# Kernel optimization log

Hardware: AMD Instinct MI355X
Metric: run time of the kernel (lower is better)

The kernel has to match this reference:

```python
import jax, jax.numpy as jnp
import numpy as np

N_NODES = 100000
N_EDGES = 1600000
D_IN = 64
HID = 64
N_GRAPHS = 256


def _glorot(key, shape):
    lim = float(np.sqrt(6.0 / (shape[0] + shape[1])))
    return jax.random.uniform(key, shape, jnp.float32, -lim, lim)


def setup_inputs() -> dict:
    key = jax.random.key(0)
    ks = jax.random.split(key, 12)
    x = jax.random.normal(ks[0], (N_NODES, D_IN), jnp.float32)
    edge_index = jax.random.randint(ks[1], (2, N_EDGES), 0, N_NODES, jnp.int64)
    batch = jnp.sort(jax.random.randint(ks[2], (N_NODES,), 0, N_GRAPHS, jnp.int64))
    params = {
        'Wrel1': _glorot(ks[3], (D_IN, HID)), 'brel1': jnp.zeros((HID,), jnp.float32), 'Wroot1': _glorot(ks[4], (D_IN, HID)),
        'Wrel2': _glorot(ks[5], (HID, HID)), 'brel2': jnp.zeros((HID,), jnp.float32), 'Wroot2': _glorot(ks[6], (HID, HID)),
        'Wrel3': _glorot(ks[7], (HID, HID)), 'brel3': jnp.zeros((HID,), jnp.float32), 'Wroot3': _glorot(ks[8], (HID, HID)),
        'Wlin': _glorot(ks[9], (HID, HID)), 'blin': jnp.zeros((HID,), jnp.float32),
    }
    return {'x': x, 'edge_index': edge_index, 'batch': batch, **params}


def _graph_conv(x, src, dst, Wrel, brel, Wroot):
    # PyG GraphConv: lin_rel(sum_{j in N(i)} x_j) + lin_root(x_i); bias on lin_rel only.
    aggr = jax.ops.segment_sum(x[src], dst, num_segments=N_NODES)  # [N, d] gather+scatter-add
    return aggr @ Wrel + brel + x @ Wroot


def reference(x, edge_index, batch, Wrel1, brel1, Wroot1, Wrel2, brel2, Wroot2,
              Wrel3, brel3, Wroot3, Wlin, blin):
    src, dst = edge_index[0], edge_index[1]
    h = jax.nn.relu(_graph_conv(x, src, dst, Wrel1, brel1, Wroot1))
    h = jax.nn.relu(_graph_conv(h, src, dst, Wrel2, brel2, Wroot2))
    h = _graph_conv(h, src, dst, Wrel3, brel3, Wroot3)
    # global_mean_pool over graphs
    sums = jax.ops.segment_sum(h, batch, num_segments=N_GRAPHS)          # [G, HID]
    counts = jax.ops.segment_sum(jnp.ones((N_NODES,), h.dtype), batch, num_segments=N_GRAPHS)
    pooled = sums / jnp.maximum(counts, 1.0)[:, None]
    # dropout is identity in eval mode
    return pooled @ Wlin + blin
```

## Files before the change

kernel.cpp:

```cpp
#include <hip/hip_runtime.h>
#include <hip/hip_bf16.h>

#define NN 100000
#define NE 1600000
#define DD 64
#define NG 256
#define SHIFT 8
#define NBK 391
#define BCAP 4608
#define NSB 256
#define CHUNK 6250

typedef __attribute__((ext_vector_type(8))) short bf16x8;
typedef __attribute__((ext_vector_type(4))) float f32x4;
typedef __attribute__((ext_vector_type(8))) unsigned short ushort8v;

__device__ __forceinline__ float b2f(ushort u){
  unsigned v = ((unsigned)u) << 16;
  return __uint_as_float(v);
}
__device__ __forceinline__ ushort f2b(float f){
  __hip_bfloat16 b = __float2bfloat16(f);
  return *(ushort*)&b;
}

__global__ void k_wpack3(const float* __restrict__ Wr1, const float* __restrict__ Wo1,
                         const float* __restrict__ Wr2, const float* __restrict__ Wo2,
                         const float* __restrict__ Wr3, const float* __restrict__ Wo3,
                         ushort* __restrict__ wp, int* __restrict__ gcur){
  int i = blockIdx.x*256 + threadIdx.x;
  if (i < NBK) gcur[i] = i*BCAP;
  if (i >= 3*8192) return;
  int lay = i >> 13;
  int r = i & 8191;
  int j = r & 7, l = (r>>3) & 63, t = (r>>9) & 7, s = r >> 12;
  int k = s*32 + ((l>>4)<<3) + j;
  int col = t*16 + (l&15);
  const float* Wrel  = (lay==0) ? Wr1 : (lay==1) ? Wr2 : Wr3;
  const float* Wroot = (lay==0) ? Wo1 : (lay==1) ? Wo2 : Wo3;
  float v = (col < 64) ? Wrel[k*64 + col] : Wroot[k*64 + (col-64)];
  wp[i] = f2b(v);
}

__global__ __launch_bounds__(256) void k_bscatter(const int* __restrict__ src, const int* __restrict__ dst,
                           int* __restrict__ gcur, unsigned* __restrict__ ebuf){
  __shared__ int h[NBK];
  __shared__ int base[NBK];
  __shared__ int lcur[NBK];
  for (int i=threadIdx.x; i<NBK; i+=256) h[i]=0;
  __syncthreads();
  const int e0 = blockIdx.x*CHUNK;
  const int e1 = min(e0+CHUNK, NE);
  for (int e=e0+threadIdx.x; e<e1; e+=256) atomicAdd(&h[dst[e]>>SHIFT], 1);
  __syncthreads();
  for (int i=threadIdx.x; i<NBK; i+=256){
    base[i] = h[i] ? atomicAdd(&gcur[i], h[i]) : 0;
    lcur[i] = 0;
  }
  __syncthreads();
  for (int e=e0+threadIdx.x; e<e1; e+=256){
    int d = dst[e];
    int b = d >> SHIFT;
    int r = atomicAdd(&lcur[b], 1);
    size_t idx = (size_t)base[b] + r;
    if (idx < (size_t)NBK*BCAP)
      ebuf[idx] = ((unsigned)(d & 255) << 17) | (unsigned)src[e];
  }
}

__global__ __launch_bounds__(256) void k_bfill(const unsigned* __restrict__ ebuf, const int* __restrict__ gcur,
                        int* __restrict__ rowptr, int* __restrict__ degarr, int* __restrict__ csr){
  __shared__ int c[256];
  __shared__ int lcur[256];
  __shared__ int s[256];
  __shared__ int scnt;
  const int b = blockIdx.x, t = threadIdx.x;
  const int ebase = b*BCAP;
  if (t == 0) scnt = min(gcur[b] - ebase, BCAP);
  c[t] = 0;
  __syncthreads();
  const int cnt = scnt;
  for (int i=t; i<cnt; i+=256) atomicAdd(&c[ebuf[ebase+i]>>17], 1);
  __syncthreads();
  int v = c[t];
  s[t] = v;
  __syncthreads();
  for (int off=1; off<256; off<<=1){
    int u = (t >= off) ? s[t-off] : 0;
    __syncthreads();
    s[t] += u;
    __syncthreads();
  }
  int excl = s[t] - v;
  lcur[t] = excl;
  int node = (b << SHIFT) + t;
  if (node < NN){ rowptr[node] = ebase + excl; degarr[node] = v; }
  __syncthreads();
  for (int i=t; i<cnt; i+=256){
    unsigned p = ebuf[ebase+i];
    int dl = (int)(p >> 17);
    int r = atomicAdd(&lcur[dl], 1);
    csr[ebase + r] = (int)(p & 0x1FFFFu);
  }
}

#define CPAD 136
__global__ __launch_bounds__(256) void k_gemm_mfma(const void* __restrict__ Av, int aIsF32,
    const ushort* __restrict__ wp, ushort* __restrict__ Y, ushort* __restrict__ Rr){
  __shared__ ushort ct[64*CPAD];
  const int tid = threadIdx.x;
  const int w = tid >> 6, l = tid & 63;
  const int m = l & 15, kg = l >> 4;
  const int row0 = blockIdx.x*64;
  int arow = row0 + w*16 + m; if (arow >= NN) arow = NN-1;
  bf16x8 a0, a1;
  if (aIsF32){
    const float* Af = (const float*)Av;
    float4 f0 = *(const float4*)&Af[(size_t)arow*64 + kg*8];
    float4 f1 = *(const float4*)&Af[(size_t)arow*64 + kg*8 + 4];
    float4 f2 = *(const float4*)&Af[(size_t)arow*64 + 32 + kg*8];
    float4 f3 = *(const float4*)&Af[(size_t)arow*64 + 32 + kg*8 + 4];
    a0[0]=(short)f2b(f0.x); a0[1]=(short)f2b(f0.y); a0[2]=(short)f2b(f0.z); a0[3]=(short)f2b(f0.w);
    a0[4]=(short)f2b(f1.x); a0[5]=(short)f2b(f1.y); a0[6]=(short)f2b(f1.z); a0[7]=(short)f2b(f1.w);
    a1[0]=(short)f2b(f2.x); a1[1]=(short)f2b(f2.y); a1[2]=(short)f2b(f2.z); a1[3]=(short)f2b(f2.w);
    a1[4]=(short)f2b(f3.x); a1[5]=(short)f2b(f3.y); a1[6]=(short)f2b(f3.z); a1[7]=(short)f2b(f3.w);
  } else {
    const ushort* Ab = (const ushort*)Av;
    a0 = *(const bf16x8*)&Ab[(size_t)arow*64 + kg*8];
    a1 = *(const bf16x8*)&Ab[(size_t)arow*64 + 32 + kg*8];
  }
  #pragma unroll
  for (int t=0; t<8; t++){
    bf16x8 b0 = *(const bf16x8*)&wp[((size_t)(0*8+t)*64 + l)*8];
    bf16x8 b1 = *(const bf16x8*)&wp[((size_t)(1*8+t)*64 + l)*8];
    f32x4 c = {0.f, 0.f, 0.f, 0.f};
    c = __builtin_amdgcn_mfma_f32_16x16x32_bf16(a0, b0, c, 0, 0, 0);
    c = __builtin_amdgcn_mfma_f32_16x16x32_bf16(a1, b1, c, 0, 0, 0);
    #pragma unroll
    for (int reg=0; reg<4; reg++){
      int lrow = w*16 + kg*4 + reg;
      ct[lrow*CPAD + t*16 + m] = f2b(c[reg]);
    }
  }
  __syncthreads();
  #pragma unroll
  for (int u=0; u<4; u++){
    int i = tid + u*256;
    int lrow = i >> 4, cb = i & 15;
    int grow = row0 + lrow;
    if (grow < NN){
      ushort8v v = *(const ushort8v*)&ct[lrow*CPAD + cb*8];
      if (cb < 8) *(ushort8v*)&Y [(size_t)grow*64 + cb*8]       = v;
      else        *(ushort8v*)&Rr[(size_t)grow*64 + (cb-8)*8]   = v;
    }
  }
}

__global__ __launch_bounds__(256) void k_aggr(const ushort* __restrict__ Y,
    const ushort* __restrict__ R, const float* __restrict__ brel,
    const int* __restrict__ rowptr, const int* __restrict__ degarr, const int* __restrict__ csr,
    ushort* __restrict__ hout, int do_relu){
  int node = blockIdx.x*4 + (threadIdx.x>>6);
  if (node >= NN) return;
  int lane = threadIdx.x & 63;
  int g = lane >> 3;
  int c8 = (lane & 7) << 3;
  int beg = rowptr[node];
  int dc = degarr[node];
  const int* lst = csr + beg;
  float a[8] = {0.f,0.f,0.f,0.f,0.f,0.f,0.f,0.f};
  int i = g;
  for (; i + 8 < dc; i += 16){
    int s0 = lst[i], s1 = lst[i+8];
    ushort8v y0 = *(const ushort8v*)&Y[((size_t)s0<<6) + c8];
    ushort8v y1 = *(const ushort8v*)&Y[((size_t)s1<<6) + c8];
    #pragma unroll
    for (int j=0;j<8;j++) a[j] += b2f(y0[j]) + b2f(y1[j]);
  }
  if (i < dc){
    int s0 = lst[i];
    ushort8v y0 = *(const ushort8v*)&Y[((size_t)s0<<6) + c8];
    #pragma unroll
    for (int j=0;j<8;j++) a[j] += b2f(y0[j]);
  }
  #pragma unroll
  for (int j=0;j<8;j++){
    a[j] += __shfl_xor(a[j], 8);
    a[j] += __shfl_xor(a[j], 16);
    a[j] += __shfl_xor(a[j], 32);
  }
  if (g == 0){
    ushort8v r8 = *(const ushort8v*)&R[((size_t)node<<6) + c8];
    float4 b0 = *(const float4*)&brel[c8];
    float4 b1 = *(const float4*)&brel[c8+4];
    float bb[8] = {b0.x,b0.y,b0.z,b0.w,b1.x,b1.y,b1.z,b1.w};
    ushort8v o;
    #pragma unroll
    for (int j=0;j<8;j++){
      float v = a[j] + b2f(r8[j]) + bb[j];
      if (do_relu) v = fmaxf(v, 0.f);
      o[j] = f2b(v);
    }
    *(ushort8v*)&hout[((size_t)node<<6) + c8] = o;
  }
}

__global__ __launch_bounds__(256) void k_pool(const ushort* __restrict__ h, const int* __restrict__ batch,
                       const float* __restrict__ Wlin, const float* __restrict__ blin,
                       float* __restrict__ out){
  int g = blockIdx.x;
  int lo=0, hi=NN;
  while (lo<hi){ int mid=(lo+hi)>>1; if (batch[mid] < g) lo=mid+1; else hi=mid; }
  int beg = lo;
  lo=0; hi=NN;
  while (lo<hi){ int mid=(lo+hi)>>1; if (batch[mid] < g+1) lo=mid+1; else hi=mid; }
  int end = lo;
  int lane = threadIdx.x & 63;
  int w = threadIdx.x >> 6;
  float acc = 0.f;
  for (int n = beg + w; n < end; n += 4) acc += b2f(h[(size_t)n*64 + lane]);
  __shared__ float red[4][64];
  __shared__ float p[64];
  red[w][lane] = acc;
  __syncthreads();
  if (w == 0){
    float v = red[0][lane]+red[1][lane]+red[2][lane]+red[3][lane];
    int cnt = end - beg;
    p[lane] = v / fmaxf((float)cnt, 1.f);
  }
  __syncthreads();
  if (w == 0){
    float o = blin[lane];
    #pragma unroll 8
    for (int k=0;k<64;k++) o += p[k]*Wlin[k*64+lane];
    out[g*64+lane] = o;
  }
}

extern "C" void kernel_launch(void* const* d_in, const int* in_sizes, int n_in,
                              void* d_out, int out_size, void* d_ws, size_t ws_size,
                              hipStream_t stream){
  const float* x     = (const float*)d_in[0];
  const int*   ei    = (const int*)  d_in[1];
  const int*   batch = (const int*)  d_in[2];
  const float* Wrel1 = (const float*)d_in[3];
  const float* brel1 = (const float*)d_in[4];
  const float* Wroot1= (const float*)d_in[5];
  const float* Wrel2 = (const float*)d_in[6];
  const float* brel2 = (const float*)d_in[7];
  const float* Wroot2= (const float*)d_in[8];
  const float* Wrel3 = (const float*)d_in[9];
  const float* brel3 = (const float*)d_in[10];
  const float* Wroot3= (const float*)d_in[11];
  const float* Wlin  = (const float*)d_in[12];
  const float* blin  = (const float*)d_in[13];
  const int* src = ei;
  const int* dst = ei + NE;

  char* wsB = (char*)d_ws;
  size_t off = 0;
  auto alloc = [&](size_t bytes)->void*{
    void* p = wsB + off; off = (off + bytes + 255) & ~(size_t)255; return p;
  };
  int*      csr    = (int*)     alloc((size_t)NBK*BCAP*4);
  unsigned* ebuf   = (unsigned*)alloc((size_t)NBK*BCAP*4);
  int*      rowptr = (int*)     alloc((size_t)NN*4);
  int*      degarr = (int*)     alloc((size_t)NN*4);
  int*      gcur   = (int*)     alloc(NBK*4);
  ushort*   wp     = (ushort*)  alloc((size_t)3*8192*2);
  ushort*   Y      = (ushort*)  alloc((size_t)NN*64*2);
  ushort*   R      = (ushort*)  alloc((size_t)NN*64*2);
  ushort*   h1     = (ushort*)  alloc((size_t)NN*64*2);
  ushort*   h2     = (ushort*)  alloc((size_t)NN*64*2);

  k_wpack3  <<<(3*8192+255)/256,256,0,stream>>>(Wrel1,Wroot1,Wrel2,Wroot2,Wrel3,Wroot3, wp, gcur);
  k_bscatter<<<NSB,256,0,stream>>>(src, dst, gcur, ebuf);
  k_bfill   <<<NBK,256,0,stream>>>(ebuf, gcur, rowptr, degarr, csr);

  int gb = (NN+63)/64;
  int ab = (NN+3)/4;

  k_gemm_mfma<<<gb,256,0,stream>>>(x,  1, wp + 0*8192, Y, R);
  k_aggr     <<<ab,256,0,stream>>>(Y, R, brel1, rowptr, degarr, csr, h1, 1);
  k_gemm_mfma<<<gb,256,0,stream>>>(h1, 0, wp + 1*8192, Y, R);
  k_aggr     <<<ab,256,0,stream>>>(Y, R, brel2, rowptr, degarr, csr, h2, 1);
  k_gemm_mfma<<<gb,256,0,stream>>>(h2, 0, wp + 2*8192, Y, R);
  k_aggr     <<<ab,256,0,stream>>>(Y, R, brel3, rowptr, degarr, csr, h1, 0);

  k_pool <<<NG,256,0,stream>>>(h1, batch, Wlin, blin, (float*)d_out);
}
```

Baseline: 251.9 us.

## Fuse aggregation with next layer's MFMA GEMM via shared-memory staging

Layers 1 and 2 now use one kernel that aggregates neighbours for a 64-node tile, applies bias and ReLU, stages the result in shared memory, and immediately runs the next layer's MFMA transform. This removes the h1/h2 round trips through global memory and two kernel launches. In exchange each block walks 16 nodes per wave in sequence, giving fewer blocks and less latency hiding for the gather. It also needs ping-pong Y/R buffers.

```diff
diff --git a/kernel.cpp b/kernel.cpp
--- a/kernel.cpp
+++ b/kernel.cpp
@@ -10,6 +10,7 @@
 #define BCAP 4608
 #define NSB 256
 #define CHUNK 6250
+#define FB 1563
 
 typedef __attribute__((ext_vector_type(8))) short bf16x8;
 typedef __attribute__((ext_vector_type(4))) float f32x4;
@@ -105,7 +106,7 @@
 }
 
 #define CPAD 136
-__global__ __launch_bounds__(256) void k_gemm_mfma(const void* __restrict__ Av, int aIsF32,
+__global__ __launch_bounds__(256) void k_gemm_mfma(const float* __restrict__ Af,
     const ushort* __restrict__ wp, ushort* __restrict__ Y, ushort* __restrict__ Rr){
   __shared__ ushort ct[64*CPAD];
   const int tid = threadIdx.x;
@@ -114,8 +115,7 @@
   const int row0 = blockIdx.x*64;
   int arow = row0 + w*16 + m; if (arow >= NN) arow = NN-1;
   bf16x8 a0, a1;
-  if (aIsF32){
-    const float* Af = (const float*)Av;
+  {
     float4 f0 = *(const float4*)&Af[(size_t)arow*64 + kg*8];
     float4 f1 = *(const float4*)&Af[(size_t)arow*64 + kg*8 + 4];
     float4 f2 = *(const float4*)&Af[(size_t)arow*64 + 32 + kg*8];
@@ -124,10 +124,6 @@
     a0[4]=(short)f2b(f1.x); a0[5]=(short)f2b(f1.y); a0[6]=(short)f2b(f1.z); a0[7]=(short)f2b(f1.w);
     a1[0]=(short)f2b(f2.x); a1[1]=(short)f2b(f2.y); a1[2]=(short)f2b(f2.z); a1[3]=(short)f2b(f2.w);
     a1[4]=(short)f2b(f3.x); a1[5]=(short)f2b(f3.y); a1[6]=(short)f2b(f3.z); a1[7]=(short)f2b(f3.w);
-  } else {
-    const ushort* Ab = (const ushort*)Av;
-    a0 = *(const bf16x8*)&Ab[(size_t)arow*64 + kg*8];
-    a1 = *(const bf16x8*)&Ab[(size_t)arow*64 + 32 + kg*8];
   }
   #pragma unroll
   for (int t=0; t<8; t++){
@@ -156,10 +152,95 @@
   }
 }
 
+__global__ __launch_bounds__(256) void k_fused(
+    const ushort* __restrict__ Y, const ushort* __restrict__ R,
+    const float* __restrict__ brel,
+    const int* __restrict__ rowptr, const int* __restrict__ degarr,
+    const int* __restrict__ csr,
+    const ushort* __restrict__ wpn, ushort* __restrict__ Yn, ushort* __restrict__ Rn){
+  __shared__ union { ushort sh[64][72]; ushort ct[64*CPAD]; } sm;
+  const int tid = threadIdx.x;
+  const int wv = tid >> 6, lane = tid & 63;
+  const int g = lane >> 3, c8 = (lane & 7) << 3;
+  const int nbase = blockIdx.x * 64;
+  for (int it = 0; it < 16; ++it){
+    int node = nbase + wv*16 + it;
+    if (node < NN){
+      int beg = rowptr[node];
+      int dc = degarr[node];
+      const int* lst = csr + beg;
+      float a[8] = {0.f,0.f,0.f,0.f,0.f,0.f,0.f,0.f};
+      int i = g;
+      for (; i + 8 < dc; i += 16){
+        int s0 = lst[i], s1 = lst[i+8];
+        ushort8v y0 = *(const ushort8v*)&Y[((size_t)s0<<6) + c8];
+        ushort8v y1 = *(const ushort8v*)&Y[((size_t)s1<<6) + c8];
+        #pragma unroll
+        for (int j=0;j<8;j++) a[j] += b2f(y0[j]) + b2f(y1[j]);
+      }
+      if (i < dc){
+        int s0 = lst[i];
+        ushort8v y0 = *(const ushort8v*)&Y[((size_t)s0<<6) + c8];
+        #pragma unroll
+        for (int j=0;j<8;j++) a[j] += b2f(y0[j]);
+      }
+      #pragma unroll
+      for (int j=0;j<8;j++){
+        a[j] += __shfl_xor(a[j], 8);
+        a[j] += __shfl_xor(a[j], 16);
+        a[j] += __shfl_xor(a[j], 32);
+      }
+      if (g == 0){
+        ushort8v r8 = *(const ushort8v*)&R[((size_t)node<<6) + c8];
+        float4 b0 = *(const float4*)&brel[c8];
+        float4 b1 = *(const float4*)&brel[c8+4];
+        float bb[8] = {b0.x,b0.y,b0.z,b0.w,b1.x,b1.y,b1.z,b1.w};
+        ushort8v o;
+        #pragma unroll
+        for (int j=0;j<8;j++){
+          float v = a[j] + b2f(r8[j]) + bb[j];
+          o[j] = f2b(fmaxf(v, 0.f));
+        }
+        *(ushort8v*)&sm.sh[wv*16 + it][c8] = o;
+      }
+    }
+  }
+  __syncthreads();
+  const int m = lane & 15, kg = lane >> 4;
+  bf16x8 a0 = *(const bf16x8*)&sm.sh[wv*16 + m][kg*8];
+  bf16x8 a1 = *(const bf16x8*)&sm.sh[wv*16 + m][32 + kg*8];
+  __syncthreads();
+  #pragma unroll
+  for (int t=0; t<8; t++){
+    bf16x8 b0 = *(const bf16x8*)&wpn[((size_t)(0*8+t)*64 + lane)*8];
+    bf16x8 b1 = *(const bf16x8*)&wpn[((size_t)(1*8+t)*64 + lane)*8];
+    f32x4 c = {0.f,0.f,0.f,0.f};
+    c = __builtin_amdgcn_mfma_f32_16x16x32_bf16(a0, b0, c, 0, 0, 0);
+    c = __builtin_amdgcn_mfma_f32_16x16x32_bf16(a1, b1, c, 0, 0, 0);
+    #pragma unroll
+    for (int reg=0; reg<4; reg++){
+      int lrow = wv*16 + kg*4 + reg;
+      sm.ct[lrow*CPAD + t*16 + m] = f2b(c[reg]);
+    }
+  }
+  __syncthreads();
+  #pragma unroll
+  for (int u=0; u<4; u++){
+    int i = tid + u*256;
+    int lrow = i >> 4, cb = i & 15;
+    int grow = nbase + lrow;
+    if (grow < NN){
+      ushort8v v = *(const ushort8v*)&sm.ct[lrow*CPAD + cb*8];
+      if (cb < 8) *(ushort8v*)&Yn[(size_t)grow*64 + cb*8]     = v;
+      else        *(ushort8v*)&Rn[(size_t)grow*64 + (cb-8)*8] = v;
+    }
+  }
+}
+
 __global__ __launch_bounds__(256) void k_aggr(const ushort* __restrict__ Y,
     const ushort* __restrict__ R, const float* __restrict__ brel,
     const int* __restrict__ rowptr, const int* __restrict__ degarr, const int* __restrict__ csr,
-    ushort* __restrict__ hout, int do_relu){
+    ushort* __restrict__ hout){
   int node = blockIdx.x*4 + (threadIdx.x>>6);
   if (node >= NN) return;
   int lane = threadIdx.x & 63;
@@ -196,11 +277,7 @@
     float bb[8] = {b0.x,b0.y,b0.z,b0.w,b1.x,b1.y,b1.z,b1.w};
     ushort8v o;
     #pragma unroll
-    for (int j=0;j<8;j++){
-      float v = a[j] + b2f(r8[j]) + bb[j];
-      if (do_relu) v = fmaxf(v, 0.f);
-      o[j] = f2b(v);
-    }
+    for (int j=0;j<8;j++) o[j] = f2b(a[j] + b2f(r8[j]) + bb[j]);
     *(ushort8v*)&hout[((size_t)node<<6) + c8] = o;
   }
 }
@@ -270,8 +347,9 @@
   ushort*   wp     = (ushort*)  alloc((size_t)3*8192*2);
   ushort*   Y      = (ushort*)  alloc((size_t)NN*64*2);
   ushort*   R      = (ushort*)  alloc((size_t)NN*64*2);
-  ushort*   h1     = (ushort*)  alloc((size_t)NN*64*2);
-  ushort*   h2     = (ushort*)  alloc((size_t)NN*64*2);
+  ushort*   Y2     = (ushort*)  alloc((size_t)NN*64*2);
+  ushort*   R2     = (ushort*)  alloc((size_t)NN*64*2);
+  ushort*   h3     = (ushort*)  alloc((size_t)NN*64*2);
 
   k_wpack3  <<<(3*8192+255)/256,256,0,stream>>>(Wrel1,Wroot1,Wrel2,Wroot2,Wrel3,Wroot3, wp, gcur);
   k_bscatter<<<NSB,256,0,stream>>>(src, dst, gcur, ebuf);
@@ -280,12 +358,10 @@
   int gb = (NN+63)/64;
   int ab = (NN+3)/4;
 
-  k_gemm_mfma<<<gb,256,0,stream>>>(x,  1, wp + 0*8192, Y, R);
-  k_aggr     <<<ab,256,0,stream>>>(Y, R, brel1, rowptr, degarr, csr, h1, 1);
-  k_gemm_mfma<<<gb,256,0,stream>>>(h1, 0, wp + 1*8192, Y, R);
-  k_aggr     <<<ab,256,0,stream>>>(Y, R, brel2, rowptr, degarr, csr, h2, 1);
-  k_gemm_mfma<<<gb,256,0,stream>>>(h2, 0, wp + 2*8192, Y, R);
-  k_aggr     <<<ab,256,0,stream>>>(Y, R, brel3, rowptr, degarr, csr, h1, 0);
-
-  k_pool <<<NG,256,0,stream>>>(h1, batch, Wlin, blin, (float*)d_out);
-}
+  k_gemm_mfma<<<gb,256,0,stream>>>(x, wp + 0*8192, Y, R);
+  k_fused   <<<FB,256,0,stream>>>(Y, R, brel1, rowptr, degarr, csr, wp + 1*8192, Y2, R2);
+  k_fused   <<<FB,256,0,stream>>>(Y2, R2, brel2, rowptr, degarr, csr, wp + 2*8192, Y, R);
+  k_aggr    <<<ab,256,0,stream>>>(Y, R, brel3, rowptr, degarr, csr, h3);
+
+  k_pool <<<NG,256,0,stream>>>(h3, batch, Wlin, blin, (float*)d_out);
+}
```

Measured after the change: 298.7 us. 1.19x slower.
